# Performance work log

Measured on AMD Instinct MI355X. Metric: run time of the kernel, lower is better.

Reference implementation:

```python
import jax, jax.numpy as jnp
import numpy as np

B, N, HID = 2, 2048, 1024
H, DH = 16, 64

def apply_rope(x, rope):
    # x: [B,H,N,D], rope: [B,N,D] interpreted as interleaved (cos, sin) pairs
    Bx, Hx, Nx, D = x.shape
    xp = x.reshape(Bx, Hx, Nx, D // 2, 2)
    rp = rope.reshape(Bx, 1, Nx, D // 2, 2)
    cos, sin = rp[..., 0], rp[..., 1]
    x0, x1 = xp[..., 0], xp[..., 1]
    out = jnp.stack([x0 * cos - x1 * sin, x1 * cos + x0 * sin], axis=-1)
    return out.reshape(Bx, Hx, Nx, D)


def setup_inputs() -> dict:
    key = jax.random.key(0)
    k1, k2, k3, k4 = jax.random.split(key, 4)
    x = jax.random.normal(k1, (B, N, HID), dtype=jnp.float32)
    rope = jax.random.normal(k2, (B, N, DH), dtype=jnp.float32)
    Wqkv = jax.random.normal(k3, (3 * H * DH, HID), dtype=jnp.float32) * (HID ** -0.5)
    Wout = jax.random.normal(k4, (HID, H * DH), dtype=jnp.float32) * ((H * DH) ** -0.5)
    return {"x": x, "rope": rope, "Wqkv": Wqkv, "Wout": Wout}


def reference(x, rope, Wqkv, Wout):
    scale = DH ** -0.5
    qkv = jnp.einsum('bnd,ed->bne', x, Wqkv)          # [B,N,3*H*DH]
    qkv = qkv.reshape(B, N, 3, H, DH)
    qkv = jnp.transpose(qkv, (2, 0, 3, 1, 4))          # [3,B,H,N,DH]
    q, k, v = qkv[0], qkv[1], qkv[2]
    q = apply_rope(q, rope)
    k = apply_rope(k, rope)
    attn = jnp.einsum('bhnd,bhmd->bhnm', q, k) * scale  # [B,H,N,N]
    attn = jax.nn.softmax(attn, axis=-1)
    out = jnp.einsum('bhnm,bhmd->bhnd', attn, v)        # [B,H,N,DH]
    out = jnp.transpose(out, (0, 2, 1, 3)).reshape(B, N, H * DH)
    return jnp.einsum('bne,de->bnd', out, Wout)
```

## Files before the change

kernel.cpp:

```cpp
#include <hip/hip_runtime.h>
#include <stdint.h>
#include <stddef.h>

typedef __bf16 bf16;
typedef __bf16 bf16x2 __attribute__((ext_vector_type(2)));
typedef __bf16 bf16x4 __attribute__((ext_vector_type(4)));
typedef __bf16 bf16x8 __attribute__((ext_vector_type(8)));
typedef float f32x2 __attribute__((ext_vector_type(2)));
typedef float f32x4 __attribute__((ext_vector_type(4)));
typedef float f32x16 __attribute__((ext_vector_type(16)));

constexpr int Bb = 2, Nn = 2048, HID = 1024, Hh = 16, DH = 64;
constexpr int MTOK = Bb * Nn;
constexpr int E3 = 3 * Hh * DH;

__global__ void cast_kernel(const float* __restrict__ in, bf16* __restrict__ out, int n4) {
  int i = blockIdx.x * blockDim.x + threadIdx.x;
  if (i >= n4) return;
  f32x4 v = reinterpret_cast<const f32x4*>(in)[i];
  bf16x4 o;
#pragma unroll
  for (int j = 0; j < 4; ++j) o[j] = (bf16)v[j];
  reinterpret_cast<bf16x4*>(out)[i] = o;
}

template <bool OUT_BF16>
__global__ __launch_bounds__(256) void gemm_bt(const bf16* __restrict__ A,
                                               const bf16* __restrict__ Bt,
                                               void* __restrict__ Cp,
                                               int M, int N, int K) {
  __shared__ __align__(16) bf16 As[128 * 32];
  __shared__ __align__(16) bf16 Bs[128 * 32];
  const int tid = threadIdx.x;
  const int lane = tid & 63;
  const int wave = tid >> 6;
  const int wr = wave >> 1, wc = wave & 1;
  const int bm = blockIdx.x, bn = blockIdx.y;
  const int frow = lane & 15;
  const int fk = (lane >> 4) * 8;
  const int c0 = wave * 128 + lane;

  f32x4 acc[4][4] = {};

  for (int k0 = 0; k0 < K; k0 += 32) {
#pragma unroll
    for (int i = 0; i < 2; ++i) {
      int c = c0 + i * 64;
      int row = c >> 2;
      int col = (c & 3) * 8;
      const bf16* ga = A + (size_t)(bm * 128 + row) * K + k0 + col;
      const bf16* gb = Bt + (size_t)(bn * 128 + row) * K + k0 + col;
      __builtin_amdgcn_global_load_lds((const __attribute__((address_space(1))) void*)ga,
                                       (__attribute__((address_space(3))) void*)(As + c * 8),
                                       16, 0, 0);
      __builtin_amdgcn_global_load_lds((const __attribute__((address_space(1))) void*)gb,
                                       (__attribute__((address_space(3))) void*)(Bs + c * 8),
                                       16, 0, 0);
    }
    __syncthreads();
    bf16x8 af[4], bfr[4];
#pragma unroll
    for (int m = 0; m < 4; ++m)
      af[m] = *reinterpret_cast<const bf16x8*>(As + (wr * 64 + m * 16 + frow) * 32 + fk);
#pragma unroll
    for (int n = 0; n < 4; ++n)
      bfr[n] = *reinterpret_cast<const bf16x8*>(Bs + (wc * 64 + n * 16 + frow) * 32 + fk);
#pragma unroll
    for (int m = 0; m < 4; ++m)
#pragma unroll
      for (int n = 0; n < 4; ++n)
        acc[m][n] = __builtin_amdgcn_mfma_f32_16x16x32_bf16(af[m], bfr[n], acc[m][n], 0, 0, 0);
    __syncthreads();
  }

  const int r0 = bm * 128 + wr * 64;
  const int cc0 = bn * 128 + wc * 64;
#pragma unroll
  for (int m = 0; m < 4; ++m)
#pragma unroll
    for (int n = 0; n < 4; ++n)
#pragma unroll
      for (int r = 0; r < 4; ++r) {
        int row = r0 + m * 16 + (lane >> 4) * 4 + r;
        int col = cc0 + n * 16 + frow;
        if (OUT_BF16)
          ((bf16*)Cp)[(size_t)row * N + col] = (bf16)acc[m][n][r];
        else
          ((float*)Cp)[(size_t)row * N + col] = acc[m][n][r];
      }
}

__device__ __forceinline__ int kappa(int a) {
  return (((a >> 2) ^ (a >> 3)) & 1) ? (a ^ 12) : a;
}

__global__ __launch_bounds__(256) void rope_pack(const bf16* __restrict__ qkvb,
                                                 const float* __restrict__ rope,
                                                 bf16* __restrict__ qpk,
                                                 bf16* __restrict__ kpk,
                                                 bf16* __restrict__ vpk) {
  __shared__ bf16 qs[128][66];
  __shared__ bf16 ks[128][66];
  __shared__ bf16 vs[128][66];
  const int bh = blockIdx.y;
  const int b = bh >> 4;
  const int h = bh & 15;
  const int n0 = blockIdx.x * 128;
  const int t = threadIdx.x;

  for (int it = 0; it < 16; ++it) {
    int p = it * 256 + t;
    int nl = p >> 5, i = p & 31;
    int n = n0 + nl;
    size_t rowbase = (size_t)(b * Nn + n);
    const bf16* src = qkvb + rowbase * E3 + h * DH + 2 * i;
    f32x2 cs = *reinterpret_cast<const f32x2*>(rope + rowbase * DH + 2 * i);
    float c = cs[0], sn = cs[1];
    bf16x2 qv = *reinterpret_cast<const bf16x2*>(src);
    bf16x2 kv = *reinterpret_cast<const bf16x2*>(src + HID);
    bf16x2 vv = *reinterpret_cast<const bf16x2*>(src + 2 * HID);
    float q0 = (float)qv[0], q1 = (float)qv[1];
    float k0 = (float)kv[0], k1 = (float)kv[1];
    qs[nl][2 * i]     = (bf16)(q0 * c - q1 * sn);
    qs[nl][2 * i + 1] = (bf16)(q1 * c + q0 * sn);
    ks[nl][2 * i]     = (bf16)(k0 * c - k1 * sn);
    ks[nl][2 * i + 1] = (bf16)(k1 * c + k0 * sn);
    vs[nl][2 * i]     = vv[0];
    vs[nl][2 * i + 1] = vv[1];
  }
  __syncthreads();

  const int lane2 = t & 63;
  const int dd = t >> 6;
  const int lo2 = lane2 & 31, hi2 = lane2 >> 5;
  const int lok = kappa(lo2);
#pragma unroll
  for (int kbq = 0; kbq < 4; ++kbq) {
    int col = dd * 16 + hi2 * 8;
    bf16x8 q8 = *reinterpret_cast<const bf16x8*>(&qs[kbq * 32 + lo2][col]);
    bf16x8 k8 = *reinterpret_cast<const bf16x8*>(&ks[kbq * 32 + lok][col]);
    size_t base = ((((size_t)bh * 64 + (n0 >> 5) + kbq) * 4 + dd) * 64 + lane2) * 8;
    *reinterpret_cast<bf16x8*>(qpk + base) = q8;
    *reinterpret_cast<bf16x8*>(kpk + base) = k8;
  }

#pragma unroll
  for (int wi = 0; wi < 4; ++wi) {
    int id = wi * 256 + t;
    int lane3 = id & 63;
    int sub = id >> 6;
    int kt = sub >> 3, dt = (sub >> 2) & 1, kbi = sub & 3;
    int lo3 = lane3 & 31, hi3 = lane3 >> 5;
    bf16x8 v8;
#pragma unroll
    for (int j = 0; j < 8; ++j)
      v8[j] = vs[kt * 64 + kbi * 16 + hi3 * 8 + j][dt * 32 + lo3];
    size_t vbase = ((((size_t)bh * 32 + (n0 >> 6) + kt) * 8 + dt * 4 + kbi) * 64 + lane3) * 8;
    *reinterpret_cast<bf16x8*>(vpk + vbase) = v8;
  }
}

__global__ __launch_bounds__(256, 2) void attn_kernel(const bf16* __restrict__ qpk,
                                                      const bf16* __restrict__ kpk,
                                                      const bf16* __restrict__ vpk,
                                                      bf16* __restrict__ outb) {
  const int lane = threadIdx.x & 63;
  const int wave = threadIdx.x >> 6;
  const int bid = blockIdx.x;
  const int xcd = bid & 7;
  const int idx = bid >> 3;
  const int bh = xcd * 4 + (idx >> 4);
  const int qt = idx & 15;
  const int b = bh >> 4, h = bh & 15;
  const int lo = lane & 31;
  const int hi = lane >> 5;
  const int q0 = qt * 128 + wave * 32;

  constexpr float SCL = 0.125f * 1.44269504088896340736f;

  bf16x8 qf[4];
#pragma unroll
  for (int d = 0; d < 4; ++d)
    qf[d] = *reinterpret_cast<const bf16x8*>(
        qpk + ((((size_t)bh * 64 + qt * 4 + wave) * 4 + d) * 64 + lane) * 8);

  f32x16 o0 = {}, o1 = {};
  float mrun = -3e38f, lrun = 0.f;

  auto cvtpk = [](float a, float b) {
    unsigned w;
    asm("v_cvt_pk_bf16_f32 %0, %1, %2" : "=v"(w) : "v"(a), "v"(b));
    return w;
  };

  auto loadK64 = [&](int key0, bf16x8* kf) {
    size_t base = (((size_t)bh * 64 + (key0 >> 5)) * 4 * 64 + lane) * 8;
#pragma unroll
    for (int half = 0; half < 2; ++half)
#pragma unroll
      for (int d = 0; d < 4; ++d)
        kf[half * 4 + d] = *reinterpret_cast<const bf16x8*>(
            kpk + base + (half * 4 + d) * 512);
  };

  auto tilestep64 = [&](int key0, const bf16x8* kf) {
    bf16x8 vf[8];
    size_t vbase = (((size_t)bh * 32 + (key0 >> 6)) * 8 * 64 + lane) * 8;
#pragma unroll
    for (int sub = 0; sub < 8; ++sub)
      vf[sub] = *reinterpret_cast<const bf16x8*>(vpk + vbase + sub * 512);

    f32x16 s0 = {}, s1 = {};
#pragma unroll
    for (int d = 0; d < 4; ++d) {
      s0 = __builtin_amdgcn_mfma_f32_32x32x16_bf16(kf[d], qf[d], s0, 0, 0, 0);
      s1 = __builtin_amdgcn_mfma_f32_32x32x16_bf16(kf[4 + d], qf[d], s1, 0, 0, 0);
    }

    float t16[16];
#pragma unroll
    for (int r = 0; r < 16; ++r) t16[r] = fmaxf(s0[r], s1[r]);
#pragma unroll
    for (int r = 0; r < 8; ++r) t16[r] = fmaxf(t16[r], t16[r + 8]);
#pragma unroll
    for (int r = 0; r < 4; ++r) t16[r] = fmaxf(t16[r], t16[r + 4]);
    float tmv = fmaxf(fmaxf(t16[0], t16[2]), fmaxf(t16[1], t16[3]));
    float tm = fmaxf(tmv, __shfl_xor(tmv, 32));
    float tms = tm * SCL;

    if (__any(tms > mrun + 8.0f)) {
      float mn = fmaxf(mrun, tms);
      float corr = __builtin_amdgcn_exp2f(mrun - mn);
      mrun = mn;
      lrun *= corr;
#pragma unroll
      for (int r = 0; r < 16; ++r) { o0[r] *= corr; o1[r] *= corr; }
    }

    float e[32];
#pragma unroll
    for (int r = 0; r < 16; ++r) e[r] = __builtin_amdgcn_exp2f(fmaf(s0[r], SCL, -mrun));
#pragma unroll
    for (int r = 0; r < 16; ++r) e[16 + r] = __builtin_amdgcn_exp2f(fmaf(s1[r], SCL, -mrun));

    float u[16];
#pragma unroll
    for (int r = 0; r < 16; ++r) u[r] = e[r] + e[16 + r];
#pragma unroll
    for (int r = 0; r < 8; ++r) u[r] += u[r + 8];
#pragma unroll
    for (int r = 0; r < 4; ++r) u[r] += u[r + 4];
    float tsv = (u[0] + u[2]) + (u[1] + u[3]);
    lrun += tsv + __shfl_xor(tsv, 32);

    union { unsigned w[4]; bf16x8 v8; } pb[4];
#pragma unroll
    for (int c = 0; c < 4; ++c)
#pragma unroll
      for (int w = 0; w < 4; ++w)
        pb[c].w[w] = cvtpk(e[c * 8 + 2 * w], e[c * 8 + 2 * w + 1]);

#pragma unroll
    for (int kbi = 0; kbi < 4; ++kbi) {
      o0 = __builtin_amdgcn_mfma_f32_32x32x16_bf16(vf[kbi], pb[kbi].v8, o0, 0, 0, 0);
      o1 = __builtin_amdgcn_mfma_f32_32x32x16_bf16(vf[4 + kbi], pb[kbi].v8, o1, 0, 0, 0);
    }
  };

  bf16x8 kA[8], kB[8];
  loadK64(0, kA);
  for (int t = 0; t < 32; t += 2) {
    loadK64((t + 1) * 64, kB);
    __builtin_amdgcn_sched_barrier(0);
    tilestep64(t * 64, kA);
    int n2 = (t + 2 < 32) ? (t + 2) * 64 : 0;
    loadK64(n2, kA);
    __builtin_amdgcn_sched_barrier(0);
    tilestep64((t + 1) * 64, kB);
  }

  float invl = 1.0f / lrun;
#pragma unroll
  for (int dt = 0; dt < 2; ++dt) {
#pragma unroll
    for (int g = 0; g < 4; ++g) {
      bf16x4 ov;
#pragma unroll
      for (int j = 0; j < 4; ++j) {
        float val = (dt ? o1[g * 4 + j] : o0[g * 4 + j]) * invl;
        ov[j] = (bf16)val;
      }
      int dh = dt * 32 + g * 8 + hi * 4;
      *reinterpret_cast<bf16x4*>(outb + (size_t)(b * Nn + q0 + lo) * HID + h * DH + dh) = ov;
    }
  }
}

extern "C" void kernel_launch(void* const* d_in, const int* in_sizes, int n_in,
                              void* d_out, int out_size, void* d_ws, size_t ws_size,
                              hipStream_t stream) {
  const float* x = (const float*)d_in[0];
  const float* rope = (const float*)d_in[1];
  const float* Wqkv = (const float*)d_in[2];
  const float* Wout = (const float*)d_in[3];
  float* out = (float*)d_out;

  char* w = (char*)d_ws;
  size_t off = 0;
  auto alloc = [&](size_t bytes) -> void* {
    void* p = w + off;
    off += (bytes + 255) & ~(size_t)255;
    return p;
  };
  bf16* xb    = (bf16*)alloc((size_t)MTOK * HID * 2);
  bf16* wqkvb = (bf16*)alloc((size_t)E3 * HID * 2);
  bf16* woutb = (bf16*)alloc((size_t)HID * HID * 2);
  bf16* qkvb  = (bf16*)alloc((size_t)MTOK * E3 * 2);
  bf16* qpk   = (bf16*)alloc((size_t)Bb * Hh * Nn * DH * 2);
  bf16* kpk   = (bf16*)alloc((size_t)Bb * Hh * Nn * DH * 2);
  bf16* vpk   = (bf16*)alloc((size_t)Bb * Hh * Nn * DH * 2);
  bf16* attno = (bf16*)alloc((size_t)MTOK * HID * 2);

  cast_kernel<<<(MTOK * HID / 4) / 256, 256, 0, stream>>>(x, xb, MTOK * HID / 4);
  cast_kernel<<<(E3 * HID / 4) / 256, 256, 0, stream>>>(Wqkv, wqkvb, E3 * HID / 4);
  cast_kernel<<<(HID * HID / 4) / 256, 256, 0, stream>>>(Wout, woutb, HID * HID / 4);

  gemm_bt<true><<<dim3(MTOK / 128, E3 / 128), 256, 0, stream>>>(xb, wqkvb, qkvb, MTOK, E3, HID);

  rope_pack<<<dim3(Nn / 128, Bb * Hh), 256, 0, stream>>>(qkvb, rope, qpk, kpk, vpk);

  attn_kernel<<<dim3(512), 256, 0, stream>>>(qpk, kpk, vpk, attno);

  gemm_bt<false><<<dim3(MTOK / 128, HID / 128), 256, 0, stream>>>(attno, woutb, out, MTOK, HID, HID);
}
```

Baseline: 140.1 us.

## Stage K/V tiles through LDS with async global_load_lds double buffering

Each workgroup's four waves now cooperatively copy each 64-key K and V tile into a double-buffered LDS region using global_load_lds, instead of every wave loading K and V from global memory into registers on its own. This cuts redundant global/L2 traffic, since the four waves of a block share the same keys, and it overlaps the next tile's load with the current tile's compute. The price is a __syncthreads per tile and extra LDS reads. The change also defers the cross-half shuffle of the row sum to the end and shuffles the max only when a rescale happens.

```diff
diff --git a/kernel.cpp b/kernel.cpp
--- a/kernel.cpp
+++ b/kernel.cpp
@@ -164,8 +164,10 @@
                                                       const bf16* __restrict__ kpk,
                                                       const bf16* __restrict__ vpk,
                                                       bf16* __restrict__ outb) {
-  const int lane = threadIdx.x & 63;
-  const int wave = threadIdx.x >> 6;
+  __shared__ __align__(16) char kvlds[2][16384];
+  const int tid = threadIdx.x;
+  const int lane = tid & 63;
+  const int wave = tid >> 6;
   const int bid = blockIdx.x;
   const int xcd = bid & 7;
   const int idx = bid >> 3;
@@ -193,22 +195,38 @@
     return w;
   };
 
-  auto loadK64 = [&](int key0, bf16x8* kf) {
-    size_t base = (((size_t)bh * 64 + (key0 >> 5)) * 4 * 64 + lane) * 8;
-#pragma unroll
-    for (int half = 0; half < 2; ++half)
-#pragma unroll
-      for (int d = 0; d < 4; ++d)
-        kf[half * 4 + d] = *reinterpret_cast<const bf16x8*>(
-            kpk + base + (half * 4 + d) * 512);
+  const bf16* kg = kpk + (size_t)bh * 131072 + wave * 512 + lane * 8;
+  const bf16* vg = vpk + (size_t)bh * 131072 + wave * 512 + lane * 8;
+
+  auto stage = [&](int til, int buf) {
+    char* ld = &kvlds[buf][wave * 1024];
+    const bf16* kk = kg + (size_t)til * 4096;
+    const bf16* vv = vg + (size_t)til * 4096;
+#pragma unroll
+    for (int i = 0; i < 2; ++i) {
+      __builtin_amdgcn_global_load_lds((const __attribute__((address_space(1))) void*)(kk + i * 2048),
+                                       (__attribute__((address_space(3))) void*)(ld + i * 4096),
+                                       16, 0, 0);
+      __builtin_amdgcn_global_load_lds((const __attribute__((address_space(1))) void*)(vv + i * 2048),
+                                       (__attribute__((address_space(3))) void*)(ld + 8192 + i * 4096),
+                                       16, 0, 0);
+    }
   };
 
-  auto tilestep64 = [&](int key0, const bf16x8* kf) {
-    bf16x8 vf[8];
-    size_t vbase = (((size_t)bh * 32 + (key0 >> 6)) * 8 * 64 + lane) * 8;
-#pragma unroll
-    for (int sub = 0; sub < 8; ++sub)
-      vf[sub] = *reinterpret_cast<const bf16x8*>(vpk + vbase + sub * 512);
+  stage(0, 0);
+  __syncthreads();
+
+  for (int t = 0; t < 32; ++t) {
+    const int cur = t & 1;
+    if (t < 31) stage(t + 1, cur ^ 1);
+
+    const char* kb = &kvlds[cur][lane * 16];
+    bf16x8 kf[8], vf[8];
+#pragma unroll
+    for (int c = 0; c < 8; ++c) {
+      kf[c] = *reinterpret_cast<const bf16x8*>(kb + c * 1024);
+      vf[c] = *reinterpret_cast<const bf16x8*>(kb + 8192 + c * 1024);
+    }
 
     f32x16 s0 = {}, s1 = {};
 #pragma unroll
@@ -225,11 +243,10 @@
 #pragma unroll
     for (int r = 0; r < 4; ++r) t16[r] = fmaxf(t16[r], t16[r + 4]);
     float tmv = fmaxf(fmaxf(t16[0], t16[2]), fmaxf(t16[1], t16[3]));
-    float tm = fmaxf(tmv, __shfl_xor(tmv, 32));
-    float tms = tm * SCL;
-
-    if (__any(tms > mrun + 8.0f)) {
-      float mn = fmaxf(mrun, tms);
+
+    if (__any(tmv * SCL > mrun + 8.0f)) {
+      float tm = fmaxf(tmv, __shfl_xor(tmv, 32));
+      float mn = fmaxf(mrun, tm * SCL);
       float corr = __builtin_amdgcn_exp2f(mrun - mn);
       mrun = mn;
       lrun *= corr;
@@ -250,8 +267,7 @@
     for (int r = 0; r < 8; ++r) u[r] += u[r + 8];
 #pragma unroll
     for (int r = 0; r < 4; ++r) u[r] += u[r + 4];
-    float tsv = (u[0] + u[2]) + (u[1] + u[3]);
-    lrun += tsv + __shfl_xor(tsv, 32);
+    lrun += (u[0] + u[2]) + (u[1] + u[3]);
 
     union { unsigned w[4]; bf16x8 v8; } pb[4];
 #pragma unroll
@@ -265,19 +281,11 @@
       o0 = __builtin_amdgcn_mfma_f32_32x32x16_bf16(vf[kbi], pb[kbi].v8, o0, 0, 0, 0);
       o1 = __builtin_amdgcn_mfma_f32_32x32x16_bf16(vf[4 + kbi], pb[kbi].v8, o1, 0, 0, 0);
     }
-  };
-
-  bf16x8 kA[8], kB[8];
-  loadK64(0, kA);
-  for (int t = 0; t < 32; t += 2) {
-    loadK64((t + 1) * 64, kB);
-    __builtin_amdgcn_sched_barrier(0);
-    tilestep64(t * 64, kA);
-    int n2 = (t + 2 < 32) ? (t + 2) * 64 : 0;
-    loadK64(n2, kA);
-    __builtin_amdgcn_sched_barrier(0);
-    tilestep64((t + 1) * 64, kB);
-  }
+
+    __syncthreads();
+  }
+
+  lrun += __shfl_xor(lrun, 32);
 
   float invl = 1.0f / lrun;
 #pragma unroll
```

After: 136.3 us. 2.7% less time.
